# Optimization experiments

Measured on AMD Instinct MI355X. Metric: run time of the kernel, lower is better.

The kernel has to match this reference:

```python
import jax, jax.numpy as jnp
import numpy as np

OUT, IN, GS = 8192, 8192, 128
N_GROUPS = OUT * IN // GS  # 524288


def setup_inputs() -> dict:
    key = jax.random.key(0)
    k1, k2, k3 = jax.random.split(key, 3)
    x = jax.random.normal(k1, (32, IN), dtype=jnp.float32)
    # ternary values in {-1, 0, 1}
    ternary = jax.random.randint(k2, (OUT, IN), -1, 2, dtype=jnp.int32)
    # positive per-group scales
    scales = jax.random.uniform(k3, (N_GROUPS,), dtype=jnp.float32, minval=0.01, maxval=0.1)
    return {"x": x, "ternary": ternary, "scales": scales}


def reference(x, ternary, scales):
    # Dequantize: each contiguous group of GS weights shares one scale.
    # scales: [n_groups] -> [n_groups, GS] -> [OUT, IN]
    scales_exp = jnp.broadcast_to(scales[:, None], (N_GROUPS, GS)).reshape(OUT, IN)
    w = ternary.astype(jnp.float32) * scales_exp  # [OUT, IN]
    # F.linear(x, w) = x @ w.T
    return jnp.einsum("ti,oi->to", x, w)
```

## Files before the change

### kernel.cpp

```cpp
#include <hip/hip_runtime.h>
#include <hip/hip_bf16.h>
#include <stdint.h>

#define OUT_DIM 8192
#define IN_DIM  8192
#define GS      128
#define MROWS   32
#define NSPLIT  8
#define PART_ELEMS (MROWS * OUT_DIM)

typedef __attribute__((ext_vector_type(8))) short bf16x8;
typedef __attribute__((ext_vector_type(4))) float f32x4;
typedef __attribute__((ext_vector_type(8))) unsigned short u16x8;

__device__ __forceinline__ unsigned short f2bf_rne(float f) {
    uint32_t v = __builtin_bit_cast(uint32_t, f);
    v += 0x7FFFu + ((v >> 16) & 1u);
    return (unsigned short)(v >> 16);
}

__global__ __launch_bounds__(256) void prep_xbf(const float* __restrict__ x,
                                                unsigned short* __restrict__ xbf) {
    int i = (blockIdx.x * 256 + threadIdx.x) * 8;
    float4 a = *(const float4*)(x + i);
    float4 b = *(const float4*)(x + i + 4);
    float f[8] = {a.x, a.y, a.z, a.w, b.x, b.y, b.z, b.w};
    u16x8 u;
#pragma unroll
    for (int j = 0; j < 8; ++j) u[j] = f2bf_rne(f[j]);
    *(u16x8*)(xbf + i) = u;
}

__global__ __launch_bounds__(256) void ternary_gemm(
    const int* __restrict__ tern, const float* __restrict__ scales,
    const unsigned short* __restrict__ xbf, float* __restrict__ part) {
    const int wave  = blockIdx.x * 4 + (threadIdx.x >> 6);
    const int lane  = threadIdx.x & 63;
    const int kc    = wave >> 9;
    const int ntile = wave & 511;
    const int n     = lane & 15;
    const int quad  = lane >> 4;
    const int o      = (ntile << 4) + n;
    const int k0base = kc << 10;

    const int* __restrict__ wrow = tern + (size_t)o * IN_DIM;
    const unsigned short* __restrict__ xr0 = xbf + n * IN_DIM;
    const unsigned short* __restrict__ xr1 = xbf + (16 + n) * IN_DIM;

    const float* __restrict__ sp = scales + o * (IN_DIM / GS) + (kc << 3);
    float s_cur = sp[0];

    f32x4 acc0 = {0.f, 0.f, 0.f, 0.f};
    f32x4 acc1 = {0.f, 0.f, 0.f, 0.f};

#pragma unroll 1
    for (int it = 0; it < 8; ++it) {
        const unsigned int p = f2bf_rne(s_cur);
        float s_nxt = sp[(it < 7) ? (it + 1) : 7];
        const int k0 = k0base + (it << 7);
#pragma unroll
        for (int st = 0; st < 4; ++st) {
            const int k = k0 + (st << 5) + (quad << 3);
            int4 w0 = *(const int4*)(wrow + k);
            int4 w1 = *(const int4*)(wrow + k + 4);
            bf16x8 a0 = *(const bf16x8*)(xr0 + k);
            bf16x8 a1 = *(const bf16x8*)(xr1 + k);
            int tw[8] = {w0.x, w0.y, w0.z, w0.w, w1.x, w1.y, w1.z, w1.w};
            bf16x8 bfr;
#pragma unroll
            for (int j = 0; j < 8; ++j) {
                int t = tw[j];
                unsigned int v = p | ((unsigned int)t & 0x8000u);
                bfr[j] = (short)((t == 0) ? 0u : v);
            }
            acc0 = __builtin_amdgcn_mfma_f32_16x16x32_bf16(a0, bfr, acc0, 0, 0, 0);
            acc1 = __builtin_amdgcn_mfma_f32_16x16x32_bf16(a1, bfr, acc1, 0, 0, 0);
        }
        s_cur = s_nxt;
    }

    float* __restrict__ prow = part + (size_t)kc * PART_ELEMS;
#pragma unroll
    for (int r = 0; r < 4; ++r) {
        prow[(quad * 4 + r) * OUT_DIM + o]        = acc0[r];
        prow[(quad * 4 + r + 16) * OUT_DIM + o]   = acc1[r];
    }
}

__global__ __launch_bounds__(256) void reduce_parts(const float* __restrict__ part,
                                                    float* __restrict__ out) {
    const int i = (blockIdx.x * 256 + threadIdx.x) * 4;
    float4 s = *(const float4*)(part + i);
#pragma unroll
    for (int kc = 1; kc < NSPLIT; ++kc) {
        float4 v = *(const float4*)(part + (size_t)kc * PART_ELEMS + i);
        s.x += v.x; s.y += v.y; s.z += v.z; s.w += v.w;
    }
    *(float4*)(out + i) = s;
}

extern "C" void kernel_launch(void* const* d_in, const int* in_sizes, int n_in,
                              void* d_out, int out_size, void* d_ws, size_t ws_size,
                              hipStream_t stream) {
    const float* x      = (const float*)d_in[0];
    const int*   tern   = (const int*)d_in[1];
    const float* scales = (const float*)d_in[2];
    float* out = (float*)d_out;

    unsigned short* xbf = (unsigned short*)d_ws;
    float* part = (float*)((char*)d_ws + (512 << 10));

    prep_xbf<<<128, 256, 0, stream>>>(x, xbf);
    ternary_gemm<<<1024, 256, 0, stream>>>(tern, scales, xbf, part);
    reduce_parts<<<256, 256, 0, stream>>>(part, out);
}
```

Baseline: 380.1 us.

## Pack ternary weights to 2 bits in a pre-pass before the GEMM

Adds a streaming kernel that packs the int32 ternary weights into 2-bit codes, 16 per uint32, in a tile-friendly order. The GEMM then reads one 32-bit word per lane per MFMA step instead of two int4 loads, and decodes sign and zero with bit operations. The intent is to turn the latency-bound GEMM into a light one and move the full-size weight read into a simple, bandwidth-efficient pass. The trade-off is an extra launch and an extra write and read of the packed buffer on every call.

```diff
diff --git a/kernel.cpp b/kernel.cpp
--- a/kernel.cpp
+++ b/kernel.cpp
@@ -8,6 +8,7 @@
 #define MROWS   32
 #define NSPLIT  8
 #define PART_ELEMS (MROWS * OUT_DIM)
+#define NPACK (OUT_DIM * IN_DIM / 16)
 
 typedef __attribute__((ext_vector_type(8))) short bf16x8;
 typedef __attribute__((ext_vector_type(4))) float f32x4;
@@ -31,19 +32,41 @@
     *(u16x8*)(xbf + i) = u;
 }
 
+__global__ __launch_bounds__(256) void compress_w(const int* __restrict__ tern,
+                                                  uint32_t* __restrict__ packed) {
+    const int g  = blockIdx.x * 256 + threadIdx.x;
+    const int r  = g & 15;
+    const int kd = (g >> 4) & 511;
+    const int T  = g >> 13;
+    const int* src = tern + (size_t)(T * 16 + r) * IN_DIM + kd * 16;
+    int4 w0 = *(const int4*)(src);
+    int4 w1 = *(const int4*)(src + 4);
+    int4 w2 = *(const int4*)(src + 8);
+    int4 w3 = *(const int4*)(src + 12);
+    int w[16] = {w0.x, w0.y, w0.z, w0.w, w1.x, w1.y, w1.z, w1.w,
+                 w2.x, w2.y, w2.z, w2.w, w3.x, w3.y, w3.z, w3.w};
+    uint32_t acc = 0;
+#pragma unroll
+    for (int j = 0; j < 16; ++j) acc |= ((uint32_t)w[j] & 3u) << (2 * j);
+    packed[g] = acc;
+}
+
 __global__ __launch_bounds__(256) void ternary_gemm(
-    const int* __restrict__ tern, const float* __restrict__ scales,
+    const uint32_t* __restrict__ packed, const float* __restrict__ scales,
     const unsigned short* __restrict__ xbf, float* __restrict__ part) {
     const int wave  = blockIdx.x * 4 + (threadIdx.x >> 6);
     const int lane  = threadIdx.x & 63;
     const int kc    = wave >> 9;
-    const int ntile = wave & 511;
+    const int T     = wave & 511;
     const int n     = lane & 15;
     const int quad  = lane >> 4;
-    const int o      = (ntile << 4) + n;
+    const int hsh   = lane & 16;
+    const int qh    = (lane >> 5) & 1;
+    const int o     = (T << 4) + n;
     const int k0base = kc << 10;
 
-    const int* __restrict__ wrow = tern + (size_t)o * IN_DIM;
+    const uint32_t* __restrict__ wp =
+        packed + (size_t)T * 8192 + kc * 1024 + qh * 16 + n;
     const unsigned short* __restrict__ xr0 = xbf + n * IN_DIM;
     const unsigned short* __restrict__ xr1 = xbf + (16 + n) * IN_DIM;
 
@@ -55,23 +78,23 @@
 
 #pragma unroll 1
     for (int it = 0; it < 8; ++it) {
-        const unsigned int p = f2bf_rne(s_cur);
+        const uint32_t p = f2bf_rne(s_cur);
         float s_nxt = sp[(it < 7) ? (it + 1) : 7];
         const int k0 = k0base + (it << 7);
+        const uint32_t* __restrict__ wit = wp + (it << 7);
 #pragma unroll
         for (int st = 0; st < 4; ++st) {
+            const uint32_t dw = wit[st << 5];
+            const uint32_t c  = dw >> hsh;
             const int k = k0 + (st << 5) + (quad << 3);
-            int4 w0 = *(const int4*)(wrow + k);
-            int4 w1 = *(const int4*)(wrow + k + 4);
             bf16x8 a0 = *(const bf16x8*)(xr0 + k);
             bf16x8 a1 = *(const bf16x8*)(xr1 + k);
-            int tw[8] = {w0.x, w0.y, w0.z, w0.w, w1.x, w1.y, w1.z, w1.w};
             bf16x8 bfr;
 #pragma unroll
             for (int j = 0; j < 8; ++j) {
-                int t = tw[j];
-                unsigned int v = p | ((unsigned int)t & 0x8000u);
-                bfr[j] = (short)((t == 0) ? 0u : v);
+                uint32_t bits = (c >> (2 * j)) & 3u;
+                uint32_t v = (p | ((bits & 2u) << 14)) & (0u - (bits & 1u));
+                bfr[j] = (short)v;
             }
             acc0 = __builtin_amdgcn_mfma_f32_16x16x32_bf16(a0, bfr, acc0, 0, 0, 0);
             acc1 = __builtin_amdgcn_mfma_f32_16x16x32_bf16(a1, bfr, acc1, 0, 0, 0);
@@ -108,9 +131,11 @@
     float* out = (float*)d_out;
 
     unsigned short* xbf = (unsigned short*)d_ws;
-    float* part = (float*)((char*)d_ws + (512 << 10));
+    float* part   = (float*)((char*)d_ws + (1u << 20));
+    uint32_t* pkd = (uint32_t*)((char*)d_ws + (16u << 20));
 
     prep_xbf<<<128, 256, 0, stream>>>(x, xbf);
-    ternary_gemm<<<1024, 256, 0, stream>>>(tern, scales, xbf, part);
+    compress_w<<<NPACK / 256, 256, 0, stream>>>(tern, pkd);
+    ternary_gemm<<<1024, 256, 0, stream>>>(pkd, scales, xbf, part);
     reduce_parts<<<256, 256, 0, stream>>>(part, out);
 }
```

Measured after the change: 395.5 us. 1.04x slower.
